# Kernel tuning notes

Measured on AMD Instinct MI355X. Metric: run time of the kernel, lower is better.

Reference implementation:

```python
import jax, jax.numpy as jnp
import numpy as np

D_MODEL = 768
N_HEADS = 12
D_FF = 3072
EPS = 1e-6


def _xavier(key, shape):
    fan_out, fan_in = shape
    a = jnp.sqrt(6.0 / (fan_in + fan_out))
    return jax.random.uniform(key, shape, jnp.float32, -a, a)


def setup_inputs() -> dict:
    key = jax.random.key(0)
    ks = jax.random.split(key, 10)
    B, S = 2, 2048
    x = jax.random.normal(ks[0], (B, S, D_MODEL), jnp.float32)
    mask = jax.random.randint(ks[1], (B, 1, 1, S), 0, 2) == 1
    wq = _xavier(ks[2], (D_MODEL, D_MODEL)); bq = jnp.zeros((D_MODEL,))
    wk = _xavier(ks[3], (D_MODEL, D_MODEL)); bk = jnp.zeros((D_MODEL,))
    wv = _xavier(ks[4], (D_MODEL, D_MODEL)); bv = jnp.zeros((D_MODEL,))
    wo = _xavier(ks[5], (D_MODEL, D_MODEL)); bo = jnp.zeros((D_MODEL,))
    w1 = _xavier(ks[6], (D_FF, D_MODEL)); b1 = jnp.zeros((D_FF,))
    w2 = _xavier(ks[7], (D_MODEL, D_FF)); b2 = jnp.zeros((D_MODEL,))
    g1 = jnp.ones((D_MODEL,)); be1 = jnp.zeros((D_MODEL,))
    g2 = jnp.ones((D_MODEL,)); be2 = jnp.zeros((D_MODEL,))
    return dict(x=x, mask=mask, wq=wq, bq=bq, wk=wk, bk=bk, wv=wv, bv=bv,
                wo=wo, bo=bo, w1=w1, b1=b1, w2=w2, b2=b2,
                g1=g1, be1=be1, g2=g2, be2=be2)


def _layer_norm(x, gamma, beta):
    # torch: mean + unbiased std (ddof=1), divide by (std + eps)
    mean = jnp.mean(x, axis=-1, keepdims=True)
    std = jnp.std(x, axis=-1, keepdims=True, ddof=1)
    return gamma * (x - mean) / (std + EPS) + beta


def _encoder(x, mask, wq, bq, wk, bk, wv, bv, wo, bo, w1, b1, w2, b2, g1, be1, g2, be2):
    B, S, D = x.shape
    H, Dk = N_HEADS, D // N_HEADS
    q = (x @ wq.T + bq).reshape(B, S, H, Dk).transpose(0, 2, 1, 3)
    k = (x @ wk.T + bk).reshape(B, S, H, Dk).transpose(0, 2, 1, 3)
    v = (x @ wv.T + bv).reshape(B, S, H, Dk).transpose(0, 2, 1, 3)
    scores = jnp.einsum('bhqd,bhkd->bhqk', q, k) / jnp.sqrt(jnp.float32(Dk))
    scores = jnp.where(mask, jnp.float32(-1e9), scores)
    probs = jax.nn.softmax(scores, axis=-1)
    attn = jnp.einsum('bhqk,bhkd->bhqd', probs, v)
    attn = attn.transpose(0, 2, 1, 3).reshape(B, S, D)
    attn = attn @ wo.T + bo
    x = _layer_norm(x + attn, g1, be1)
    ff = jax.nn.relu(x @ w1.T + b1) @ w2.T + b2
    return _layer_norm(x + ff, g2, be2)


def reference(x, mask, wq, bq, wk, bk, wv, bv, wo, bo, w1, b1, w2, b2, g1, be1, g2, be2):
    return _encoder(x, mask, wq, bq, wk, bk, wv, bv, wo, bo, w1, b1, w2, b2, g1, be1, g2, be2)
```

## Files before the change

kernel.cpp:

```cpp
#include <hip/hip_runtime.h>
#include <hip/hip_bf16.h>

typedef __hip_bfloat16 bf16;
typedef unsigned short ushort;
typedef __attribute__((ext_vector_type(8))) short short8;
typedef __attribute__((ext_vector_type(4))) float f32x4;

__device__ __forceinline__ float b2f(bf16 h) { return __bfloat162float(h); }
__device__ __forceinline__ bf16 f2b(float f) { return __float2bfloat16(f); }
__device__ __forceinline__ ushort f2bu(float f) {
    bf16 t = __float2bfloat16(f);
    ushort u;
    __builtin_memcpy(&u, &t, 2);
    return u;
}
__device__ __forceinline__ float bits2f(unsigned int u16) {
    unsigned int v = u16 << 16;
    float f;
    __builtin_memcpy(&f, &v, 4);
    return f;
}

template <typename T> __device__ __forceinline__ float toF(T v);
template <> __device__ __forceinline__ float toF<bf16>(bf16 v) { return b2f(v); }
template <> __device__ __forceinline__ float toF<float>(float v) { return v; }

template <typename T> __device__ __forceinline__ T fromF(float v);
template <> __device__ __forceinline__ bf16 fromF<bf16>(float v) { return f2b(v); }
template <> __device__ __forceinline__ float fromF<float>(float v) { return v; }

template <typename T> __device__ __forceinline__ void load8f(const T* p, float* f);
template <> __device__ __forceinline__ void load8f<bf16>(const bf16* p, float* f) {
    uint4 u = *(const uint4*)p;
    f[0] = bits2f(u.x & 0xffffu); f[1] = bits2f(u.x >> 16);
    f[2] = bits2f(u.y & 0xffffu); f[3] = bits2f(u.y >> 16);
    f[4] = bits2f(u.z & 0xffffu); f[5] = bits2f(u.z >> 16);
    f[6] = bits2f(u.w & 0xffffu); f[7] = bits2f(u.w >> 16);
}
template <> __device__ __forceinline__ void load8f<float>(const float* p, float* f) {
    float4 a = *(const float4*)p;
    float4 b = *(const float4*)(p + 4);
    f[0] = a.x; f[1] = a.y; f[2] = a.z; f[3] = a.w;
    f[4] = b.x; f[5] = b.y; f[6] = b.z; f[7] = b.w;
}

__device__ __forceinline__ void gload16(const void* g, void* l) {
    __builtin_amdgcn_global_load_lds(
        (const __attribute__((address_space(1))) void*)g,
        (__attribute__((address_space(3))) void*)l, 16, 0, 0);
}

__global__ void detect_dtype_kernel(const unsigned short* __restrict__ x,
                                    int* __restrict__ flag) {
    __shared__ int cnt;
    if (threadIdx.x == 0) cnt = 0;
    __syncthreads();
    int local = 0;
    for (int i = threadIdx.x; i < 2048; i += 256) {
        float v = bits2f((unsigned int)x[i]);
        if (!(fabsf(v) < 1e4f)) local++;
    }
    atomicAdd(&cnt, local);
    __syncthreads();
    if (threadIdx.x == 0) flag[0] = (cnt >= 8) ? 1 : 0;
}

template <typename T>
__global__ __launch_bounds__(256) void conv_x_k(
    const int* __restrict__ dflag, int want,
    const T* __restrict__ x, ushort* __restrict__ xb)
{
    if (dflag[0] != want) return;
    const int gt = blockIdx.x * 256 + threadIdx.x;
    const int stride = gridDim.x * 256;
    for (int v = gt; v < 393216; v += stride) {
        float f[8];
        load8f<T>(x + (size_t)v * 8, f);
        unsigned int wd[4];
        #pragma unroll
        for (int i = 0; i < 4; ++i)
            wd[i] = (unsigned int)f2bu(f[2 * i]) | ((unsigned int)f2bu(f[2 * i + 1]) << 16);
        *(uint4*)(xb + (size_t)v * 8) = make_uint4(wd[0], wd[1], wd[2], wd[3]);
    }
}

template <typename T>
__global__ __launch_bounds__(256) void conv_w_k(
    const int* __restrict__ dflag, int want,
    const T* __restrict__ wq, const T* __restrict__ wk, const T* __restrict__ wv,
    const T* __restrict__ wo, const T* __restrict__ w1, const T* __restrict__ w2,
    const T* __restrict__ bq, const T* __restrict__ bk, const T* __restrict__ bv,
    const T* __restrict__ bo, const T* __restrict__ b1, const T* __restrict__ b2,
    const T* __restrict__ g1, const T* __restrict__ be1,
    const T* __restrict__ g2, const T* __restrict__ be2,
    ushort* __restrict__ wall, float* __restrict__ vall)
{
    if (dflag[0] != want) return;
    const int gt = blockIdx.x * 256 + threadIdx.x;
    const int stride = gridDim.x * 256;
    for (int v = gt; v < 884736; v += stride) {
        const T* src; int loc;
        if (v < 73728)        { src = wq; loc = v; }
        else if (v < 147456)  { src = wk; loc = v - 73728; }
        else if (v < 221184)  { src = wv; loc = v - 147456; }
        else if (v < 294912)  { src = wo; loc = v - 221184; }
        else if (v < 589824)  { src = w1; loc = v - 294912; }
        else                  { src = w2; loc = v - 589824; }
        float f[8];
        load8f<T>(src + (size_t)loc * 8, f);
        unsigned int wd[4];
        #pragma unroll
        for (int i = 0; i < 4; ++i)
            wd[i] = (unsigned int)f2bu(f[2 * i]) | ((unsigned int)f2bu(f[2 * i + 1]) << 16);
        *(uint4*)(wall + (size_t)v * 8) = make_uint4(wd[0], wd[1], wd[2], wd[3]);
    }
    for (int i = gt; i < 9984; i += stride) {
        const T* s; int l;
        if (i < 768)       { s = bq;  l = i; }
        else if (i < 1536) { s = bk;  l = i - 768; }
        else if (i < 2304) { s = bv;  l = i - 1536; }
        else if (i < 3072) { s = bo;  l = i - 2304; }
        else if (i < 6144) { s = b1;  l = i - 3072; }
        else if (i < 6912) { s = b2;  l = i - 6144; }
        else if (i < 7680) { s = g1;  l = i - 6912; }
        else if (i < 8448) { s = be1; l = i - 7680; }
        else if (i < 9216) { s = g2;  l = i - 8448; }
        else               { s = be2; l = i - 9216; }
        vall[i] = toF<T>(s[l]);
    }
}

template <int BM>
__device__ __forceinline__ void gemm_bf16_body(
    const ushort* __restrict__ A, const ushort* __restrict__ Bw,
    const float* __restrict__ bias, ushort* __restrict__ Cb,
    float* __restrict__ Cf, int N, int K, int bm, int bn, int relu)
{
    __shared__ __align__(16) ushort As[BM][32];
    __shared__ __align__(16) ushort Bs[128][32];
    const int tid = threadIdx.x;
    const int w = tid >> 6, lane = tid & 63;
    const int quad = lane >> 4, l15 = lane & 15;
    constexpr int FM = BM / 32;
    const int wr = (w >> 1) * (BM / 2), wc = (w & 1) * 64;

    constexpr int CA = (BM * 64) / 4096;
    size_t aoff[CA]; int albase[CA];
    #pragma unroll
    for (int c = 0; c < CA; ++c) {
        int byte = c * 4096 + w * 1024 + lane * 16;
        int row = byte >> 6, cs = (byte >> 4) & 3;
        aoff[c] = (size_t)(bm + row) * K + cs * 8;
        albase[c] = c * 4096 + w * 1024;
    }
    size_t boff[2]; int blbase[2];
    #pragma unroll
    for (int c = 0; c < 2; ++c) {
        int byte = c * 4096 + w * 1024 + lane * 16;
        int row = byte >> 6, cs = (byte >> 4) & 3;
        boff[c] = (size_t)(bn + row) * K + cs * 8;
        blbase[c] = c * 4096 + w * 1024;
    }

    f32x4 acc[FM][4];
    #pragma unroll
    for (int i = 0; i < FM; ++i)
        #pragma unroll
        for (int j = 0; j < 4; ++j) acc[i][j] = (f32x4){0.f, 0.f, 0.f, 0.f};

    char* AsB = (char*)&As[0][0];
    char* BsB = (char*)&Bs[0][0];

    for (int k0 = 0; k0 < K; k0 += 32) {
        __syncthreads();
        #pragma unroll
        for (int c = 0; c < CA; ++c)
            gload16(A + aoff[c] + k0, AsB + albase[c]);
        #pragma unroll
        for (int c = 0; c < 2; ++c)
            gload16(Bw + boff[c] + k0, BsB + blbase[c]);
        __syncthreads();

        short8 af[FM], bfr[4];
        #pragma unroll
        for (int i = 0; i < FM; ++i)
            af[i] = *(const short8*)&As[wr + i * 16 + l15][quad * 8];
        #pragma unroll
        for (int j = 0; j < 4; ++j)
            bfr[j] = *(const short8*)&Bs[wc + j * 16 + l15][quad * 8];
        #pragma unroll
        for (int i = 0; i < FM; ++i)
            #pragma unroll
            for (int j = 0; j < 4; ++j)
                acc[i][j] = __builtin_amdgcn_mfma_f32_16x16x32_bf16(
                    af[i], bfr[j], acc[i][j], 0, 0, 0);
    }

    #pragma unroll
    for (int j = 0; j < 4; ++j) {
        int col = bn + wc + j * 16 + l15;
        float bv = bias[col];
        #pragma unroll
        for (int i = 0; i < FM; ++i) {
            int row0 = bm + wr + i * 16 + quad * 4;
            #pragma unroll
            for (int r = 0; r < 4; ++r) {
                float vv = acc[i][j][r] + bv;
                if (relu) vv = fmaxf(vv, 0.f);
                size_t idx = (size_t)(row0 + r) * N + col;
                if (Cb) Cb[idx] = f2bu(vv);
                if (Cf) Cf[idx] = vv;
            }
        }
    }
}

template <int BM>
__global__ __launch_bounds__(256) void gemm_b(
    const ushort* __restrict__ A, const ushort* __restrict__ Bw,
    const float* __restrict__ bias, ushort* __restrict__ Cb,
    float* __restrict__ Cf, int N, int K, int relu)
{
    gemm_bf16_body<BM>(A, Bw, bias, Cb, Cf, N, K,
                       blockIdx.y * BM, blockIdx.x * 128, relu);
}

__global__ __launch_bounds__(256) void gemm_qkv_b(
    const ushort* __restrict__ x, const ushort* __restrict__ wall,
    const float* __restrict__ vall,
    ushort* __restrict__ qb, ushort* __restrict__ kb, ushort* __restrict__ vb)
{
    const int mat = blockIdx.x / 6;
    const int bn = (blockIdx.x % 6) * 128;
    const ushort* W = wall + (size_t)mat * 589824;
    const float* Bi = vall + mat * 768;
    ushort* O = (mat == 0) ? qb : (mat == 1) ? kb : vb;
    gemm_bf16_body<128>(x, W, Bi, O, nullptr, 768, 768, blockIdx.y * 128, bn, 0);
}

__global__ __launch_bounds__(512) void attn_mfma_b(
    const ushort* __restrict__ q, const ushort* __restrict__ k,
    const ushort* __restrict__ v, const int* __restrict__ mask,
    float* __restrict__ opart, float* __restrict__ mlbuf)
{
    const int S = 2048, D = 768;
    const size_t NXD = 3145728;
    const float SC2 = 0.125f * 1.44269504088896f;
    __shared__ __align__(16) ushort Ks[64][72];
    __shared__ __align__(16) ushort Vt[64][72];
    __shared__ __align__(16) ushort Ps[8][16][72];
    __shared__ float mk[64];

    const int tid = threadIdx.x;
    const int w = tid >> 6, lane = tid & 63;
    const int quad = lane >> 4, l15 = lane & 15;

    const int bx = blockIdx.x;
    const int part = bx / 384;
    const int rest = bx - part * 384;
    const int q0 = (rest & 15) * 128;
    const int h = (rest >> 4) % 12;
    const int b = rest / 192;

    const size_t qrow = (size_t)(b * S + q0 + w * 16 + l15) * D + h * 64;
    const short8 aQ0 = *(const short8*)&q[qrow + quad * 8];
    const short8 aQ1 = *(const short8*)&q[qrow + 32 + quad * 8];

    short8 ones;
    #pragma unroll
    for (int j = 0; j < 8; ++j) ones[j] = (short)0x3F80;

    f32x4 o[4], lacc;
    #pragma unroll
    for (int i = 0; i < 4; ++i) o[i] = (f32x4){0.f, 0.f, 0.f, 0.f};
    lacc = (f32x4){0.f, 0.f, 0.f, 0.f};
    float m_run = -3.0e38f;

    const int sr = tid >> 3;
    const int sc0 = (tid & 7) * 8;

    uint4 ka, va;
    int mskv = 0;
    const int kbase = part * 1024;

    {
        const size_t krow = (size_t)(b * S + kbase + sr) * D + h * 64 + sc0;
        ka = *(const uint4*)&k[krow];
        const size_t vrow = (size_t)(b * S + kbase + lane) * D + h * 64 + w * 8;
        va = *(const uint4*)&v[vrow];
        if (tid < 64) mskv = mask[b * S + kbase + tid];
    }

    for (int kt = 0; kt < 16; ++kt) {
        __syncthreads();
        *(uint4*)&Ks[sr][sc0] = ka;
        {
            alignas(16) ushort tmp[8];
            *(uint4*)tmp = va;
            #pragma unroll
            for (int i = 0; i < 8; ++i) Vt[w * 8 + i][lane] = tmp[i];
        }
        if (tid < 64) mk[tid] = mskv ? -30000.f : 0.f;
        __syncthreads();

        if (kt + 1 < 16) {
            const int kk1 = kbase + (kt + 1) * 64;
            const size_t krow = (size_t)(b * S + kk1 + sr) * D + h * 64 + sc0;
            ka = *(const uint4*)&k[krow];
            const size_t vrow = (size_t)(b * S + kk1 + lane) * D + h * 64 + w * 8;
            va = *(const uint4*)&v[vrow];
            if (tid < 64) mskv = mask[b * S + kk1 + tid];
        }

        float scv[4][4];
        float vm = -3.0e38f;
        #pragma unroll
        for (int s = 0; s < 4; ++s) {
            short8 bk0 = *(const short8*)&Ks[s * 16 + l15][quad * 8];
            short8 bk1 = *(const short8*)&Ks[s * 16 + l15][32 + quad * 8];
            f32x4 c = (f32x4){0.f, 0.f, 0.f, 0.f};
            c = __builtin_amdgcn_mfma_f32_16x16x32_bf16(aQ0, bk0, c, 0, 0, 0);
            c = __builtin_amdgcn_mfma_f32_16x16x32_bf16(aQ1, bk1, c, 0, 0, 0);
            float mb = mk[s * 16 + l15];
            #pragma unroll
            for (int r = 0; r < 4; ++r) {
                float val = __builtin_fmaf(c[r], SC2, mb);
                scv[s][r] = val;
                vm = fmaxf(vm, val);
            }
        }
        vm = fmaxf(vm, __shfl_xor(vm, 1, 16));
        vm = fmaxf(vm, __shfl_xor(vm, 2, 16));
        vm = fmaxf(vm, __shfl_xor(vm, 4, 16));
        vm = fmaxf(vm, __shfl_xor(vm, 8, 16));

        if (__any(vm > m_run + 11.0f)) {
            float mn = fmaxf(m_run, vm);
            float alpha = exp2f(m_run - mn);
            #pragma unroll
            for (int s = 0; s < 4; ++s) o[s] *= alpha;
            lacc *= alpha;
            m_run = mn;
        }

        #pragma unroll
        for (int r = 0; r < 4; ++r)
            #pragma unroll
            for (int s = 0; s < 4; ++s)
                Ps[w][quad * 4 + r][(s * 16 + l15) ^ (quad << 4)] =
                    f2bu(exp2f(scv[s][r] - m_run));
        asm volatile("s_waitcnt lgkmcnt(0)" ::: "memory");

        {
            const int pswz = (l15 >> 2) << 4;
            short8 aP0 = *(const short8*)&Ps[w][l15][(quad * 8) ^ pswz];
            short8 aP1 = *(const short8*)&Ps[w][l15][(32 + quad * 8) ^ pswz];
            lacc = __builtin_amdgcn_mfma_f32_16x16x32_bf16(aP0, ones, lacc, 0, 0, 0);
            lacc = __builtin_amdgcn_mfma_f32_16x16x32_bf16(aP1, ones, lacc, 0, 0, 0);
            #pragma unroll
            for (int s = 0; s < 4; ++s) {
                short8 bv0 = *(const short8*)&Vt[s * 16 + l15][quad * 8];
                short8 bv1 = *(const short8*)&Vt[s * 16 + l15][32 + quad * 8];
                o[s] = __builtin_amdgcn_mfma_f32_16x16x32_bf16(aP0, bv0, o[s], 0, 0, 0);
                o[s] = __builtin_amdgcn_mfma_f32_16x16x32_bf16(aP1, bv1, o[s], 0, 0, 0);
            }
        }
    }

    const size_t obase = (size_t)part * NXD +
                         (size_t)(b * S + q0 + w * 16) * D + h * 64;
    #pragma unroll
    for (int r = 0; r < 4; ++r)
        #pragma unroll
        for (int s = 0; s < 4; ++s)
            opart[obase + (size_t)(quad * 4 + r) * D + s * 16 + l15] = o[s][r];
    if (l15 == 0) {
        #pragma unroll
        for (int r = 0; r < 4; ++r) {
            int row = b * S + q0 + w * 16 + quad * 4 + r;
            size_t mi = (((size_t)part * 4096 + row) * 12 + h) * 2;
            mlbuf[mi] = m_run;
            mlbuf[mi + 1] = lacc[r];
        }
    }
}

__global__ __launch_bounds__(256) void attn_combine(
    const float* __restrict__ opart, const float* __restrict__ mlbuf,
    ushort* __restrict__ ctx)
{
    const size_t NXD = 3145728;
    const int row = blockIdx.x;
    const int tid = threadIdx.x;
    #pragma unroll
    for (int i = 0; i < 3; ++i) {
        int d = tid + i * 256;
        int h = d >> 6;
        size_t m0i = ((size_t)row * 12 + h) * 2;
        size_t m1i = (((size_t)4096 + row) * 12 + h) * 2;
        float m0 = mlbuf[m0i], l0 = mlbuf[m0i + 1];
        float m1 = mlbuf[m1i], l1 = mlbuf[m1i + 1];
        float m = fmaxf(m0, m1);
        float e0 = exp2f(m0 - m), e1 = exp2f(m1 - m);
        float inv = 1.f / (l0 * e0 + l1 * e1);
        size_t idx = (size_t)row * 768 + d;
        float val = (opart[idx] * e0 + opart[NXD + idx] * e1) * inv;
        ctx[idx] = f2bu(val);
    }
}

template <typename T>
__global__ __launch_bounds__(256) void ln1_kernel(
    const int* __restrict__ dflag, int want,
    const T* __restrict__ xa, const float* __restrict__ r,
    const float* __restrict__ gamma, const float* __restrict__ beta,
    ushort* __restrict__ outb, float* __restrict__ outf)
{
    if (dflag[0] != want) return;
    const int row = blockIdx.x;
    const int tid = threadIdx.x;
    __shared__ float red[4];
    const size_t base = (size_t)row * 768;

    float x[3];
    #pragma unroll
    for (int i = 0; i < 3; ++i) {
        int d = tid + i * 256;
        x[i] = toF<T>(xa[base + d]) + r[base + d];
    }

    float s = x[0] + x[1] + x[2];
    #pragma unroll
    for (int off = 32; off > 0; off >>= 1) s += __shfl_down(s, off, 64);
    if ((tid & 63) == 0) red[tid >> 6] = s;
    __syncthreads();
    float mean = (red[0] + red[1] + red[2] + red[3]) * (1.f / 768.f);
    __syncthreads();

    float vsum = 0.f;
    #pragma unroll
    for (int i = 0; i < 3; ++i) {
        float dd = x[i] - mean;
        vsum += dd * dd;
    }
    #pragma unroll
    for (int off = 32; off > 0; off >>= 1) vsum += __shfl_down(vsum, off, 64);
    if ((tid & 63) == 0) red[tid >> 6] = vsum;
    __syncthreads();
    float var = (red[0] + red[1] + red[2] + red[3]) * (1.f / 767.f);
    float inv = 1.f / (sqrtf(var) + 1e-6f);

    #pragma unroll
    for (int i = 0; i < 3; ++i) {
        int d = tid + i * 256;
        float y = gamma[d] * (x[i] - mean) * inv + beta[d];
        outb[base + d] = f2bu(y);
        outf[base + d] = y;
    }
}

template <typename T>
__global__ __launch_bounds__(256) void ln2_kernel(
    const int* __restrict__ dflag, int want,
    const float* __restrict__ a, const float* __restrict__ r,
    const float* __restrict__ gamma, const float* __restrict__ beta,
    T* __restrict__ out)
{
    if (dflag[0] != want) return;
    const int row = blockIdx.x;
    const int tid = threadIdx.x;
    __shared__ float red[4];
    const size_t base = (size_t)row * 768;

    float x[3];
    #pragma unroll
    for (int i = 0; i < 3; ++i) {
        int d = tid + i * 256;
        x[i] = a[base + d] + r[base + d];
    }

    float s = x[0] + x[1] + x[2];
    #pragma unroll
    for (int off = 32; off > 0; off >>= 1) s += __shfl_down(s, off, 64);
    if ((tid & 63) == 0) red[tid >> 6] = s;
    __syncthreads();
    float mean = (red[0] + red[1] + red[2] + red[3]) * (1.f / 768.f);
    __syncthreads();

    float vsum = 0.f;
    #pragma unroll
    for (int i = 0; i < 3; ++i) {
        float dd = x[i] - mean;
        vsum += dd * dd;
    }
    #pragma unroll
    for (int off = 32; off > 0; off >>= 1) vsum += __shfl_down(vsum, off, 64);
    if ((tid & 63) == 0) red[tid >> 6] = vsum;
    __syncthreads();
    float var = (red[0] + red[1] + red[2] + red[3]) * (1.f / 767.f);
    float inv = 1.f / (sqrtf(var) + 1e-6f);

    #pragma unroll
    for (int i = 0; i < 3; ++i) {
        int d = tid + i * 256;
        out[base + d] = fromF<T>(gamma[d] * (x[i] - mean) * inv + beta[d]);
    }
}

extern "C" void kernel_launch(void* const* d_in, const int* in_sizes, int n_in,
                              void* d_out, int out_size, void* d_ws, size_t ws_size,
                              hipStream_t stream) {
    const size_t nxd = 3145728;
    char* base = (char*)d_ws;
    int* dflag = (int*)base;

    char* p = base + 256;
    ushort* xb   = (ushort*)p; p += nxd * 2;
    ushort* wall = (ushort*)p; p += 7077888ull * 2;
    float*  vall = (float*)p;  p += 40960;
    ushort* qb   = (ushort*)p;
    ushort* kb   = qb + nxd;
    ushort* vb   = kb + nxd;
    ushort* ctx  = vb + nxd;
    ushort* ff1b = qb;
    p += 4 * nxd * 2;
    float* oproj = (float*)p;
    float* ff2f  = oproj;
    p += nxd * 4;
    ushort* ln1b = (ushort*)p; p += nxd * 2;
    float*  ln1f = (float*)p;  p += nxd * 4;

    float* opart = oproj;
    float* mlbuf = oproj + 2 * nxd;

    const int* mask = (const int*)d_in[1];
    dim3 blk(256);

    detect_dtype_kernel<<<dim3(1), blk, 0, stream>>>(
        (const unsigned short*)d_in[0], dflag);

    conv_x_k<bf16><<<dim3(512), blk, 0, stream>>>(dflag, 0, (const bf16*)d_in[0], xb);
    conv_x_k<float><<<dim3(512), blk, 0, stream>>>(dflag, 1, (const float*)d_in[0], xb);

    conv_w_k<bf16><<<dim3(1024), blk, 0, stream>>>(dflag, 0,
        (const bf16*)d_in[2], (const bf16*)d_in[4], (const bf16*)d_in[6],
        (const bf16*)d_in[8], (const bf16*)d_in[10], (const bf16*)d_in[12],
        (const bf16*)d_in[3], (const bf16*)d_in[5], (const bf16*)d_in[7],
        (const bf16*)d_in[9], (const bf16*)d_in[11], (const bf16*)d_in[13],
        (const bf16*)d_in[14], (const bf16*)d_in[15],
        (const bf16*)d_in[16], (const bf16*)d_in[17], wall, vall);
    conv_w_k<float><<<dim3(1024), blk, 0, stream>>>(dflag, 1,
        (const float*)d_in[2], (const float*)d_in[4], (const float*)d_in[6],
        (const float*)d_in[8], (const float*)d_in[10], (const float*)d_in[12],
        (const float*)d_in[3], (const float*)d_in[5], (const float*)d_in[7],
        (const float*)d_in[9], (const float*)d_in[11], (const float*)d_in[13],
        (const float*)d_in[14], (const float*)d_in[15],
        (const float*)d_in[16], (const float*)d_in[17], wall, vall);

    gemm_qkv_b<<<dim3(18, 32), blk, 0, stream>>>(xb, wall, vall, qb, kb, vb);

    attn_mfma_b<<<dim3(768), dim3(512), 0, stream>>>(qb, kb, vb, mask, opart, mlbuf);
    attn_combine<<<dim3(4096), blk, 0, stream>>>(opart, mlbuf, ctx);

    gemm_b<64><<<dim3(6, 64), blk, 0, stream>>>(
        ctx, wall + 1769472, vall + 2304, nullptr, oproj, 768, 768, 0);

    ln1_kernel<bf16><<<dim3(4096), blk, 0, stream>>>(dflag, 0,
        (const bf16*)d_in[0], oproj, vall + 6912, vall + 7680, ln1b, ln1f);
    ln1_kernel<float><<<dim3(4096), blk, 0, stream>>>(dflag, 1,
        (const float*)d_in[0], oproj, vall + 6912, vall + 7680, ln1b, ln1f);

    gemm_b<128><<<dim3(24, 32), blk, 0, stream>>>(
        ln1b, wall + 2359296, vall + 3072, ff1b, nullptr, 3072, 768, 1);

    gemm_b<64><<<dim3(6, 64), blk, 0, stream>>>(
        ff1b, wall + 4718592, vall + 6144, nullptr, ff2f, 768, 3072, 0);

    ln2_kernel<bf16><<<dim3(4096), blk, 0, stream>>>(dflag, 0,
        ln1f, ff2f, vall + 8448, vall + 9216, (bf16*)d_out);
    ln2_kernel<float><<<dim3(4096), blk, 0, stream>>>(dflag, 1,
        ln1f, ff2f, vall + 8448, vall + 9216, (float*)d_out);
}
```

Baseline: 357.5 us.

## Widen GEMM K-tile with swizzled LDS, XCD-swizzle blocks, merge dtype-dispatch launches

The GEMM body now stages 64-wide K tiles instead of 32, with an XOR swizzle on LDS columns to avoid bank conflicts, halving the number of barrier pairs per K loop. GEMM block indices are remapped so neighbouring tiles land on the same XCD for L2 reuse. The separate bf16/float templated conversion and layernorm kernels are merged into single runtime-dispatched kernels, cutting empty launches. The attention kernel preloads the whole mask slice into shared memory once rather than per key tile. The trade-off is more LDS per GEMM block, which may lower occupancy.

Measured after the change: 332.7 us. -7.0%, faster.

```diff
diff --git a/kernel.cpp b/kernel.cpp
--- a/kernel.cpp
+++ b/kernel.cpp
@@ -21,29 +21,6 @@
     return f;
 }
 
-template <typename T> __device__ __forceinline__ float toF(T v);
-template <> __device__ __forceinline__ float toF<bf16>(bf16 v) { return b2f(v); }
-template <> __device__ __forceinline__ float toF<float>(float v) { return v; }
-
-template <typename T> __device__ __forceinline__ T fromF(float v);
-template <> __device__ __forceinline__ bf16 fromF<bf16>(float v) { return f2b(v); }
-template <> __device__ __forceinline__ float fromF<float>(float v) { return v; }
-
-template <typename T> __device__ __forceinline__ void load8f(const T* p, float* f);
-template <> __device__ __forceinline__ void load8f<bf16>(const bf16* p, float* f) {
-    uint4 u = *(const uint4*)p;
-    f[0] = bits2f(u.x & 0xffffu); f[1] = bits2f(u.x >> 16);
-    f[2] = bits2f(u.y & 0xffffu); f[3] = bits2f(u.y >> 16);
-    f[4] = bits2f(u.z & 0xffffu); f[5] = bits2f(u.z >> 16);
-    f[6] = bits2f(u.w & 0xffffu); f[7] = bits2f(u.w >> 16);
-}
-template <> __device__ __forceinline__ void load8f<float>(const float* p, float* f) {
-    float4 a = *(const float4*)p;
-    float4 b = *(const float4*)(p + 4);
-    f[0] = a.x; f[1] = a.y; f[2] = a.z; f[3] = a.w;
-    f[4] = b.x; f[5] = b.y; f[6] = b.z; f[7] = b.w;
-}
-
 __device__ __forceinline__ void gload16(const void* g, void* l) {
     __builtin_amdgcn_global_load_lds(
         (const __attribute__((address_space(1))) void*)g,
@@ -65,41 +42,55 @@
     if (threadIdx.x == 0) flag[0] = (cnt >= 8) ? 1 : 0;
 }
 
-template <typename T>
-__global__ __launch_bounds__(256) void conv_x_k(
-    const int* __restrict__ dflag, int want,
-    const T* __restrict__ x, ushort* __restrict__ xb)
-{
-    if (dflag[0] != want) return;
+__device__ __forceinline__ void load8f_rt(const void* p, int isf, float* f) {
+    if (isf) {
+        const float* q = (const float*)p;
+        float4 a = *(const float4*)q;
+        float4 b = *(const float4*)(q + 4);
+        f[0] = a.x; f[1] = a.y; f[2] = a.z; f[3] = a.w;
+        f[4] = b.x; f[5] = b.y; f[6] = b.z; f[7] = b.w;
+    } else {
+        uint4 u = *(const uint4*)p;
+        f[0] = bits2f(u.x & 0xffffu); f[1] = bits2f(u.x >> 16);
+        f[2] = bits2f(u.y & 0xffffu); f[3] = bits2f(u.y >> 16);
+        f[4] = bits2f(u.z & 0xffffu); f[5] = bits2f(u.z >> 16);
+        f[6] = bits2f(u.w & 0xffffu); f[7] = bits2f(u.w >> 16);
+    }
+}
+__device__ __forceinline__ float loadf_rt(const void* p, int isf, size_t i) {
+    return isf ? ((const float*)p)[i] : bits2f(((const ushort*)p)[i]);
+}
+
+__global__ __launch_bounds__(256) void conv_all_k(
+    const int* __restrict__ dflag,
+    const void* __restrict__ x,
+    const void* __restrict__ wq, const void* __restrict__ wk,
+    const void* __restrict__ wv, const void* __restrict__ wo,
+    const void* __restrict__ w1, const void* __restrict__ w2,
+    const void* __restrict__ bq, const void* __restrict__ bk,
+    const void* __restrict__ bv, const void* __restrict__ bo,
+    const void* __restrict__ b1, const void* __restrict__ b2,
+    const void* __restrict__ g1, const void* __restrict__ be1,
+    const void* __restrict__ g2, const void* __restrict__ be2,
+    ushort* __restrict__ xb, ushort* __restrict__ wall,
+    float* __restrict__ vall)
+{
+    const int isf = dflag[0];
+    const int esz = isf ? 4 : 2;
     const int gt = blockIdx.x * 256 + threadIdx.x;
     const int stride = gridDim.x * 256;
+
     for (int v = gt; v < 393216; v += stride) {
         float f[8];
-        load8f<T>(x + (size_t)v * 8, f);
+        load8f_rt((const char*)x + (size_t)v * 8 * esz, isf, f);
         unsigned int wd[4];
         #pragma unroll
         for (int i = 0; i < 4; ++i)
             wd[i] = (unsigned int)f2bu(f[2 * i]) | ((unsigned int)f2bu(f[2 * i + 1]) << 16);
         *(uint4*)(xb + (size_t)v * 8) = make_uint4(wd[0], wd[1], wd[2], wd[3]);
     }
-}
-
-template <typename T>
-__global__ __launch_bounds__(256) void conv_w_k(
-    const int* __restrict__ dflag, int want,
-    const T* __restrict__ wq, const T* __restrict__ wk, const T* __restrict__ wv,
-    const T* __restrict__ wo, const T* __restrict__ w1, const T* __restrict__ w2,
-    const T* __restrict__ bq, const T* __restrict__ bk, const T* __restrict__ bv,
-    const T* __restrict__ bo, const T* __restrict__ b1, const T* __restrict__ b2,
-    const T* __restrict__ g1, const T* __restrict__ be1,
-    const T* __restrict__ g2, const T* __restrict__ be2,
-    ushort* __restrict__ wall, float* __restrict__ vall)
-{
-    if (dflag[0] != want) return;
-    const int gt = blockIdx.x * 256 + threadIdx.x;
-    const int stride = gridDim.x * 256;
     for (int v = gt; v < 884736; v += stride) {
-        const T* src; int loc;
+        const void* src; int loc;
         if (v < 73728)        { src = wq; loc = v; }
         else if (v < 147456)  { src = wk; loc = v - 73728; }
         else if (v < 221184)  { src = wv; loc = v - 147456; }
@@ -107,7 +98,7 @@
         else if (v < 589824)  { src = w1; loc = v - 294912; }
         else                  { src = w2; loc = v - 589824; }
         float f[8];
-        load8f<T>(src + (size_t)loc * 8, f);
+        load8f_rt((const char*)src + (size_t)loc * 8 * esz, isf, f);
         unsigned int wd[4];
         #pragma unroll
         for (int i = 0; i < 4; ++i)
@@ -115,7 +106,7 @@
         *(uint4*)(wall + (size_t)v * 8) = make_uint4(wd[0], wd[1], wd[2], wd[3]);
     }
     for (int i = gt; i < 9984; i += stride) {
-        const T* s; int l;
+        const void* s; int l;
         if (i < 768)       { s = bq;  l = i; }
         else if (i < 1536) { s = bk;  l = i - 768; }
         else if (i < 2304) { s = bv;  l = i - 1536; }
@@ -126,7 +117,7 @@
         else if (i < 8448) { s = be1; l = i - 7680; }
         else if (i < 9216) { s = g2;  l = i - 8448; }
         else               { s = be2; l = i - 9216; }
-        vall[i] = toF<T>(s[l]);
+        vall[i] = loadf_rt(s, isf, l);
     }
 }
 
@@ -136,29 +127,32 @@
     const float* __restrict__ bias, ushort* __restrict__ Cb,
     float* __restrict__ Cf, int N, int K, int bm, int bn, int relu)
 {
-    __shared__ __align__(16) ushort As[BM][32];
-    __shared__ __align__(16) ushort Bs[128][32];
+    __shared__ __align__(16) ushort As[BM][64];
+    __shared__ __align__(16) ushort Bs[128][64];
     const int tid = threadIdx.x;
     const int w = tid >> 6, lane = tid & 63;
     const int quad = lane >> 4, l15 = lane & 15;
     constexpr int FM = BM / 32;
     const int wr = (w >> 1) * (BM / 2), wc = (w & 1) * 64;
 
-    constexpr int CA = (BM * 64) / 4096;
+    constexpr int CA = (BM * 128) / 4096;
+    constexpr int CB = 4;
     size_t aoff[CA]; int albase[CA];
     #pragma unroll
     for (int c = 0; c < CA; ++c) {
-        int byte = c * 4096 + w * 1024 + lane * 16;
-        int row = byte >> 6, cs = (byte >> 4) & 3;
-        aoff[c] = (size_t)(bm + row) * K + cs * 8;
+        int byte = c * 4096 + tid * 16;
+        int row = byte >> 7, colb = byte & 127;
+        int csrc = colb ^ ((row & 7) << 4);
+        aoff[c] = (size_t)(bm + row) * K + (csrc >> 1);
         albase[c] = c * 4096 + w * 1024;
     }
-    size_t boff[2]; int blbase[2];
-    #pragma unroll
-    for (int c = 0; c < 2; ++c) {
-        int byte = c * 4096 + w * 1024 + lane * 16;
-        int row = byte >> 6, cs = (byte >> 4) & 3;
-        boff[c] = (size_t)(bn + row) * K + cs * 8;
+    size_t boff[CB]; int blbase[CB];
+    #pragma unroll
+    for (int c = 0; c < CB; ++c) {
+        int byte = c * 4096 + tid * 16;
+        int row = byte >> 7, colb = byte & 127;
+        int csrc = colb ^ ((row & 7) << 4);
+        boff[c] = (size_t)(bn + row) * K + (csrc >> 1);
         blbase[c] = c * 4096 + w * 1024;
     }
 
@@ -171,29 +165,39 @@
     char* AsB = (char*)&As[0][0];
     char* BsB = (char*)&Bs[0][0];
 
-    for (int k0 = 0; k0 < K; k0 += 32) {
+    for (int k0 = 0; k0 < K; k0 += 64) {
         __syncthreads();
         #pragma unroll
         for (int c = 0; c < CA; ++c)
             gload16(A + aoff[c] + k0, AsB + albase[c]);
         #pragma unroll
-        for (int c = 0; c < 2; ++c)
+        for (int c = 0; c < CB; ++c)
             gload16(Bw + boff[c] + k0, BsB + blbase[c]);
         __syncthreads();
 
-        short8 af[FM], bfr[4];
-        #pragma unroll
-        for (int i = 0; i < FM; ++i)
-            af[i] = *(const short8*)&As[wr + i * 16 + l15][quad * 8];
-        #pragma unroll
-        for (int j = 0; j < 4; ++j)
-            bfr[j] = *(const short8*)&Bs[wc + j * 16 + l15][quad * 8];
-        #pragma unroll
-        for (int i = 0; i < FM; ++i)
-            #pragma unroll
-            for (int j = 0; j < 4; ++j)
-                acc[i][j] = __builtin_amdgcn_mfma_f32_16x16x32_bf16(
-                    af[i], bfr[j], acc[i][j], 0, 0, 0);
+        short8 af[FM][2], bfr[4][2];
+        #pragma unroll
+        for (int i = 0; i < FM; ++i) {
+            int r = wr + i * 16 + l15;
+            int sw = (r & 7) << 3;
+            af[i][0] = *(const short8*)&As[r][(quad * 8) ^ sw];
+            af[i][1] = *(const short8*)&As[r][(32 + quad * 8) ^ sw];
+        }
+        #pragma unroll
+        for (int j = 0; j < 4; ++j) {
+            int r = wc + j * 16 + l15;
+            int sw = (r & 7) << 3;
+            bfr[j][0] = *(const short8*)&Bs[r][(quad * 8) ^ sw];
+            bfr[j][1] = *(const short8*)&Bs[r][(32 + quad * 8) ^ sw];
+        }
+        #pragma unroll
+        for (int h = 0; h < 2; ++h)
+            #pragma unroll
+            for (int i = 0; i < FM; ++i)
+                #pragma unroll
+                for (int j = 0; j < 4; ++j)
+                    acc[i][j] = __builtin_amdgcn_mfma_f32_16x16x32_bf16(
+                        af[i][h], bfr[j][h], acc[i][j], 0, 0, 0);
     }
 
     #pragma unroll
@@ -215,14 +219,21 @@
     }
 }
 
+__device__ __forceinline__ int xcd_swz(int bid, int nwg) {
+    int cpx = nwg >> 3;
+    return (bid & 7) * cpx + (bid >> 3);
+}
+
 template <int BM>
 __global__ __launch_bounds__(256) void gemm_b(
     const ushort* __restrict__ A, const ushort* __restrict__ Bw,
     const float* __restrict__ bias, ushort* __restrict__ Cb,
     float* __restrict__ Cf, int N, int K, int relu)
 {
-    gemm_bf16_body<BM>(A, Bw, bias, Cb, Cf, N, K,
-                       blockIdx.y * BM, blockIdx.x * 128, relu);
+    int nwg = gridDim.x * gridDim.y;
+    int bid = xcd_swz(blockIdx.y * gridDim.x + blockIdx.x, nwg);
+    int bx = bid % gridDim.x, by = bid / gridDim.x;
+    gemm_bf16_body<BM>(A, Bw, bias, Cb, Cf, N, K, by * BM, bx * 128, relu);
 }
 
 __global__ __launch_bounds__(256) void gemm_qkv_b(
@@ -230,12 +241,14 @@
     const float* __restrict__ vall,
     ushort* __restrict__ qb, ushort* __restrict__ kb, ushort* __restrict__ vb)
 {
-    const int mat = blockIdx.x / 6;
-    const int bn = (blockIdx.x % 6) * 128;
+    int bid = xcd_swz(blockIdx.y * 18 + blockIdx.x, 576);
+    int bx = bid % 18, by = bid / 18;
+    const int mat = bx / 6;
+    const int bn = (bx % 6) * 128;
     const ushort* W = wall + (size_t)mat * 589824;
     const float* Bi = vall + mat * 768;
     ushort* O = (mat == 0) ? qb : (mat == 1) ? kb : vb;
-    gemm_bf16_body<128>(x, W, Bi, O, nullptr, 768, 768, blockIdx.y * 128, bn, 0);
+    gemm_bf16_body<128>(x, W, Bi, O, nullptr, 768, 768, by * 128, bn, 0);
 }
 
 __global__ __launch_bounds__(512) void attn_mfma_b(
@@ -249,7 +262,7 @@
     __shared__ __align__(16) ushort Ks[64][72];
     __shared__ __align__(16) ushort Vt[64][72];
     __shared__ __align__(16) ushort Ps[8][16][72];
-    __shared__ float mk[64];
+    __shared__ float mkAll[1024];
 
     const int tid = threadIdx.x;
     const int w = tid >> 6, lane = tid & 63;
@@ -261,6 +274,13 @@
     const int q0 = (rest & 15) * 128;
     const int h = (rest >> 4) % 12;
     const int b = rest / 192;
+    const int kbase = part * 1024;
+
+    #pragma unroll
+    for (int i = 0; i < 2; ++i) {
+        int idx = tid + i * 512;
+        mkAll[idx] = mask[b * S + kbase + idx] ? -30000.f : 0.f;
+    }
 
     const size_t qrow = (size_t)(b * S + q0 + w * 16 + l15) * D + h * 64;
     const short8 aQ0 = *(const short8*)&q[qrow + quad * 8];
@@ -279,17 +299,10 @@
     const int sr = tid >> 3;
     const int sc0 = (tid & 7) * 8;
 
-    uint4 ka, va;
-    int mskv = 0;
-    const int kbase = part * 1024;
-
-    {
-        const size_t krow = (size_t)(b * S + kbase + sr) * D + h * 64 + sc0;
-        ka = *(const uint4*)&k[krow];
-        const size_t vrow = (size_t)(b * S + kbase + lane) * D + h * 64 + w * 8;
-        va = *(const uint4*)&v[vrow];
-        if (tid < 64) mskv = mask[b * S + kbase + tid];
-    }
+    const ushort* kp = k + (size_t)(b * S + kbase + sr) * D + h * 64 + sc0;
+    const ushort* vp = v + (size_t)(b * S + kbase + lane) * D + h * 64 + w * 8;
+    uint4 ka = *(const uint4*)kp;
+    uint4 va = *(const uint4*)vp;
 
     for (int kt = 0; kt < 16; ++kt) {
         __syncthreads();
@@ -300,18 +313,16 @@
             #pragma unroll
             for (int i = 0; i < 8; ++i) Vt[w * 8 + i][lane] = tmp[i];
         }
-        if (tid < 64) mk[tid] = mskv ? -30000.f : 0.f;
         __syncthreads();
 
         if (kt + 1 < 16) {
-            const int kk1 = kbase + (kt + 1) * 64;
-            const size_t krow = (size_t)(b * S + kk1 + sr) * D + h * 64 + sc0;
-            ka = *(const uint4*)&k[krow];
-            const size_t vrow = (size_t)(b * S + kk1 + lane) * D + h * 64 + w * 8;
-            va = *(const uint4*)&v[vrow];
-            if (tid < 64) mskv = mask[b * S + kk1 + tid];
-        }
-
+            kp += 64 * D;
+            vp += 64 * D;
+            ka = *(const uint4*)kp;
+            va = *(const uint4*)vp;
+        }
+
+        const float* mk = &mkAll[kt * 64];
         float scv[4][4];
         float vm = -3.0e38f;
         #pragma unroll
@@ -409,14 +420,13 @@
     }
 }
 
-template <typename T>
 __global__ __launch_bounds__(256) void ln1_kernel(
-    const int* __restrict__ dflag, int want,
-    const T* __restrict__ xa, const float* __restrict__ r,
+    const int* __restrict__ dflag,
+    const void* __restrict__ xa, const float* __restrict__ r,
     const float* __restrict__ gamma, const float* __restrict__ beta,
     ushort* __restrict__ outb, float* __restrict__ outf)
 {
-    if (dflag[0] != want) return;
+    const int isf = dflag[0];
     const int row = blockIdx.x;
     const int tid = threadIdx.x;
     __shared__ float red[4];
@@ -426,7 +436,7 @@
     #pragma unroll
     for (int i = 0; i < 3; ++i) {
         int d = tid + i * 256;
-        x[i] = toF<T>(xa[base + d]) + r[base + d];
+        x[i] = loadf_rt(xa, isf, base + d) + r[base + d];
     }
 
     float s = x[0] + x[1] + x[2];
@@ -459,14 +469,13 @@
     }
 }
 
-template <typename T>
 __global__ __launch_bounds__(256) void ln2_kernel(
-    const int* __restrict__ dflag, int want,
+    const int* __restrict__ dflag,
     const float* __restrict__ a, const float* __restrict__ r,
     const float* __restrict__ gamma, const float* __restrict__ beta,
-    T* __restrict__ out)
-{
-    if (dflag[0] != want) return;
+    void* __restrict__ out)
+{
+    const int isf = dflag[0];
     const int row = blockIdx.x;
     const int tid = threadIdx.x;
     __shared__ float red[4];
@@ -503,7 +512,9 @@
     #pragma unroll
     for (int i = 0; i < 3; ++i) {
         int d = tid + i * 256;
-        out[base + d] = fromF<T>(gamma[d] * (x[i] - mean) * inv + beta[d]);
+        float y = gamma[d] * (x[i] - mean) * inv + beta[d];
+        if (isf) ((float*)out)[base + d] = y;
+        else     ((ushort*)out)[base + d] = f2bu(y);
     }
 }
 
@@ -539,23 +550,10 @@
     detect_dtype_kernel<<<dim3(1), blk, 0, stream>>>(
         (const unsigned short*)d_in[0], dflag);
 
-    conv_x_k<bf16><<<dim3(512), blk, 0, stream>>>(dflag, 0, (const bf16*)d_in[0], xb);
-    conv_x_k<float><<<dim3(512), blk, 0, stream>>>(dflag, 1, (const float*)d_in[0], xb);
-
-    conv_w_k<bf16><<<dim3(1024), blk, 0, stream>>>(dflag, 0,
-        (const bf16*)d_in[2], (const bf16*)d_in[4], (const bf16*)d_in[6],
-        (const bf16*)d_in[8], (const bf16*)d_in[10], (const bf16*)d_in[12],
-        (const bf16*)d_in[3], (const bf16*)d_in[5], (const bf16*)d_in[7],
-        (const bf16*)d_in[9], (const bf16*)d_in[11], (const bf16*)d_in[13],
-        (const bf16*)d_in[14], (const bf16*)d_in[15],
-        (const bf16*)d_in[16], (const bf16*)d_in[17], wall, vall);
-    conv_w_k<float><<<dim3(1024), blk, 0, stream>>>(dflag, 1,
-        (const float*)d_in[2], (const float*)d_in[4], (const float*)d_in[6],
-        (const float*)d_in[8], (const float*)d_in[10], (const float*)d_in[12],
-        (const float*)d_in[3], (const float*)d_in[5], (const float*)d_in[7],
-        (const float*)d_in[9], (const float*)d_in[11], (const float*)d_in[13],
-        (const float*)d_in[14], (const float*)d_in[15],
-        (const float*)d_in[16], (const float*)d_in[17], wall, vall);
+    conv_all_k<<<dim3(1024), blk, 0, stream>>>(dflag,
+        d_in[0], d_in[2], d_in[4], d_in[6], d_in[8], d_in[10], d_in[12],
+        d_in[3], d_in[5], d_in[7], d_in[9], d_in[11], d_in[13],
+        d_in[14], d_in[15], d_in[16], d_in[17], xb, wall, vall);
 
     gemm_qkv_b<<<dim3(18, 32), blk, 0, stream>>>(xb, wall, vall, qb, kb, vb);
 
@@ -565,10 +563,8 @@
     gemm_b<64><<<dim3(6, 64), blk, 0, stream>>>(
         ctx, wall + 1769472, vall + 2304, nullptr, oproj, 768, 768, 0);
 
-    ln1_kernel<bf16><<<dim3(4096), blk, 0, stream>>>(dflag, 0,
-        (const bf16*)d_in[0], oproj, vall + 6912, vall + 7680, ln1b, ln1f);
-    ln1_kernel<float><<<dim3(4096), blk, 0, stream>>>(dflag, 1,
-        (const float*)d_in[0], oproj, vall + 6912, vall + 7680, ln1b, ln1f);
+    ln1_kernel<<<dim3(4096), blk, 0, stream>>>(dflag,
+        d_in[0], oproj, vall + 6912, vall + 7680, ln1b, ln1f);
 
     gemm_b<128><<<dim3(24, 32), blk, 0, stream>>>(
         ln1b, wall + 2359296, vall + 3072, ff1b, nullptr, 3072, 768, 1);
@@ -576,8 +572,6 @@
     gemm_b<64><<<dim3(6, 64), blk, 0, stream>>>(
         ff1b, wall + 4718592, vall + 6144, nullptr, ff2f, 768, 3072, 0);
 
-    ln2_kernel<bf16><<<dim3(4096), blk, 0, stream>>>(dflag, 0,
-        ln1f, ff2f, vall + 8448, vall + 9216, (bf16*)d_out);
-    ln2_kernel<float><<<dim3(4096), blk, 0, stream>>>(dflag, 1,
-        ln1f, ff2f, vall + 8448, vall + 9216, (float*)d_out);
-}
+    ln2_kernel<<<dim3(4096), blk, 0, stream>>>(dflag,
+        ln1f, ff2f, vall + 8448, vall + 9216, d_out);
+}
```
